# Optimization experiments

Hardware: AMD Instinct MI355X
Metric: run time of the kernel (lower is better)

Reference implementation:

```python
import jax, jax.numpy as jnp
import numpy as np

B, C, T = 16, 192, 4096
K = 5
L = 16


def conv1d(x, w, b, pad):
    # x: [B, Cin, T], w: [Cout, Cin, K] -> [B, Cout, T]
    y = jax.lax.conv_general_dilated(
        x, w, window_strides=(1,), padding=[(pad, pad)],
        dimension_numbers=("NCH", "OIH", "NCH"))
    return y + b[None, :, None]


def setup_inputs() -> dict:
    key = jax.random.key(0)
    ks = jax.random.split(key, 8)
    scale = 0.1
    x = jax.random.normal(ks[0], (B, C, T), dtype=jnp.float32)
    mask = jnp.ones((B, 1, T), dtype=jnp.float32)
    # in_layers: Conv1d(C -> 2C, K), stacked over layers (weight-norm folded)
    W_in = jax.random.normal(ks[1], (L, 2 * C, C, K), dtype=jnp.float32) * scale
    b_in = jax.random.normal(ks[2], (L, 2 * C), dtype=jnp.float32) * scale
    # res_skip layers 0..L-2: Conv1d(C -> 2C, 1)
    W_rs = jax.random.normal(ks[3], (L - 1, 2 * C, C, 1), dtype=jnp.float32) * scale
    b_rs = jax.random.normal(ks[4], (L - 1, 2 * C), dtype=jnp.float32) * scale
    # last res_skip layer: Conv1d(C -> C, 1)
    W_last = jax.random.normal(ks[5], (C, C, 1), dtype=jnp.float32) * scale
    b_last = jax.random.normal(ks[6], (C,), dtype=jnp.float32) * scale
    return {"x": x, "mask": mask, "W_in": W_in, "b_in": b_in,
            "W_rs": W_rs, "b_rs": b_rs, "W_last": W_last, "b_last": b_last}


def reference(x, mask, W_in, b_in, W_rs, b_rs, W_last, b_last):
    pad = K // 2  # dilation_rate == 1, so padding is 'same'
    o = jnp.zeros_like(x)
    for i in range(L):
        x_in = conv1d(x, W_in[i], b_in[i], pad)          # [B, 2C, T]
        x1, x2 = x_in[:, :C], x_in[:, C:]
        acts = jnp.tanh(x1) * jax.nn.sigmoid(x2)          # gated activation (dropout=0)
        if i == L - 1:
            o = o + conv1d(acts, W_last, b_last, 0)
        else:
            rs = conv1d(acts, W_rs[i], b_rs[i], 0)        # [B, 2C, T]
            x = (x + rs[:, :C]) * mask                    # residual
            o = o + rs[:, C:]                              # skip
    return o * mask
```

## Files before the change

kernel.cpp:

```cpp
#include <hip/hip_runtime.h>
#include <hip/hip_bf16.h>

#define C 192
#define T 4096
#define L 16
#define BATCH 16
#define NT 64
#define XR 72
#define CPAD 200

#define CONV_TAP_STRIDE 73728
#define MT_STRIDE       3072
#define ICC_STRIDE      512

typedef __attribute__((ext_vector_type(8))) _Float16 half8;
typedef __attribute__((ext_vector_type(4))) _Float16 half4;
typedef __attribute__((ext_vector_type(4))) float f32x4;

__device__ __forceinline__ float gatefn(float x1, float x2) {
    float ax = fabsf(x1);
    float e  = __expf(-2.f * ax);
    float th = __builtin_copysignf((1.f - e) / (1.f + e), x1);
    float sg = 1.f / (1.f + __expf(-x2));
    return th * sg;
}

__global__ __launch_bounds__(256)
void fmt_win(const float* __restrict__ W, _Float16* __restrict__ dst, int total) {
    int gid = blockIdx.x * 256 + threadIdx.x;
    if (gid >= total) return;
    int lane = gid & 63; int r = gid >> 6;
    int icc = r % 6; r /= 6;
    int mt  = r % 24; r /= 24;
    int tap = r % 5;  int l = r / 5;
    int oc  = mt * 16 + (lane & 15);
    int ic0 = icc * 32 + (lane >> 4) * 8;
    const float* s = W + ((size_t)((l * 384 + oc) * 192 + ic0)) * 5 + tap;
    half8 v;
    #pragma unroll
    for (int i = 0; i < 8; ++i) v[i] = (_Float16)s[(size_t)i * 5];
    *reinterpret_cast<half8*>(dst + (size_t)gid * 8) = v;
}

__global__ __launch_bounds__(256)
void fmt_w11(const float* __restrict__ W, _Float16* __restrict__ dst, int mtc, int total) {
    int gid = blockIdx.x * 256 + threadIdx.x;
    if (gid >= total) return;
    int lane = gid & 63; int r = gid >> 6;
    int icc = r % 6; r /= 6;
    int mt  = r % mtc; int l = r / mtc;
    int oc  = mt * 16 + (lane & 15);
    int ic0 = icc * 32 + (lane >> 4) * 8;
    const float* s = W + (size_t)(l * (mtc * 16) + oc) * 192 + ic0;
    half8 v;
    #pragma unroll
    for (int i = 0; i < 8; ++i) v[i] = (_Float16)s[i];
    *reinterpret_cast<half8*>(dst + (size_t)gid * 8) = v;
}

__global__ __launch_bounds__(256)
void xpose(const float* __restrict__ x, _Float16* __restrict__ xh, _Float16* __restrict__ xl)
{
    __shared__ float tile[C][65];
    const int t0 = blockIdx.x * 64;
    const int b  = blockIdx.y;
    const float* xg = x + (size_t)b * C * T;
    for (int idx = threadIdx.x; idx < C * 16; idx += 256) {
        int ch = idx & 15, c = idx >> 4;
        f32x4 v = *reinterpret_cast<const f32x4*>(xg + (size_t)c * T + t0 + ch * 4);
        #pragma unroll
        for (int q = 0; q < 4; ++q) tile[c][ch * 4 + q] = v[q];
    }
    __syncthreads();
    for (int idx = threadIdx.x; idx < 64 * 24; idx += 256) {
        int cc = idx % 24, t = idx / 24;
        half8 h8, l8;
        #pragma unroll
        for (int i = 0; i < 8; ++i) {
            float v = tile[cc * 8 + i][t];
            _Float16 h = (_Float16)v;
            h8[i] = h;
            l8[i] = (_Float16)(v - (float)h);
        }
        size_t off = (size_t)b * T * C + (size_t)(t0 + t) * C + cc * 8;
        *reinterpret_cast<half8*>(xh + off) = h8;
        *reinterpret_cast<half8*>(xl + off) = l8;
    }
}

template<bool FIRST, bool LAST>
__global__ __launch_bounds__(256, 2)
void wnet_layer(const _Float16* __restrict__ xhin, const _Float16* __restrict__ xlin,
                _Float16* __restrict__ xhout, _Float16* __restrict__ xlout,
                const float* __restrict__ mask,
                const _Float16* __restrict__ wc,
                const float* __restrict__ bc,
                const _Float16* __restrict__ wr,
                const float* __restrict__ br,
                float* __restrict__ o)
{
    __shared__ __align__(16) _Float16 xhi[XR * CPAD];
    __shared__ __align__(16) _Float16 xlo[NT * CPAD];

    const int tid = threadIdx.x;
    const int t0  = blockIdx.x * NT;
    const int b   = blockIdx.y;

    {
        const _Float16* gh = xhin + (size_t)b * T * C;
        for (int idx = tid; idx < XR * 24; idx += 256) {
            int chunk = idx % 24;
            int r     = idx / 24;
            int t = t0 - 4 + r;
            half8 v = {};
            if (t >= 0 && t < T)
                v = *reinterpret_cast<const half8*>(gh + (size_t)t * C + chunk * 8);
            *reinterpret_cast<half8*>(&xhi[r * CPAD + chunk * 8]) = v;
        }
        if constexpr (!LAST) {
            const _Float16* gl = xlin + (size_t)b * T * C;
            for (int idx = tid; idx < NT * 24; idx += 256) {
                int chunk = idx % 24;
                int r     = idx / 24;
                half8 v = *reinterpret_cast<const half8*>(
                    gl + (size_t)(t0 + r) * C + chunk * 8);
                *reinterpret_cast<half8*>(&xlo[r * CPAD + chunk * 8]) = v;
            }
        }
    }
    __syncthreads();

    const int lane = tid & 63;
    const int wm   = tid >> 6;
    const int col  = lane & 15;
    const int sg   = lane >> 4;

    int wbase[6];
    #pragma unroll
    for (int q = 0; q < 6; ++q) {
        int h = q / 3, j = q % 3;
        int mt = h * 12 + wm * 3 + j;
        wbase[q] = mt * MT_STRIDE + lane * 8;
    }

    f32x4 acc[3][2][4];
    #pragma unroll
    for (int j = 0; j < 3; ++j)
    #pragma unroll
    for (int h = 0; h < 2; ++h) {
        f32x4 bv = *reinterpret_cast<const f32x4*>(bc + (h * 12 + wm * 3 + j) * 16 + sg * 4);
        #pragma unroll
        for (int p = 0; p < 4; ++p) acc[j][h][p] = bv;
    }

    half8 hA[6], hB[6];
    #pragma unroll
    for (int q = 0; q < 6; ++q)
        hA[q] = *reinterpret_cast<const half8*>(wc + wbase[q]);

    auto convstep = [&](int icc, half8 (&curH)[6], half8 (&nxtH)[6],
                        size_t tapoff, size_t ntapoff, int tap) {
        const size_t coff = tapoff + (size_t)icc * ICC_STRIDE;
        const size_t noff = (icc == 5) ? ntapoff : coff + ICC_STRIDE;
        #pragma unroll
        for (int q = 0; q < 6; ++q)
            nxtH[q] = *reinterpret_cast<const half8*>(wc + noff + wbase[q]);
        half8 bh[4];
        #pragma unroll
        for (int p = 0; p < 4; ++p) {
            int off = (p * 16 + col + tap + 2) * CPAD + icc * 32 + sg * 8;
            bh[p] = *reinterpret_cast<const half8*>(&xhi[off]);
        }
        __builtin_amdgcn_sched_barrier(0);
        __builtin_amdgcn_s_setprio(1);
        #pragma unroll
        for (int h = 0; h < 2; ++h)
        #pragma unroll
        for (int j = 0; j < 3; ++j)
        #pragma unroll
        for (int p = 0; p < 4; ++p)
            acc[j][h][p] = __builtin_amdgcn_mfma_f32_16x16x32_f16(
                curH[h * 3 + j], bh[p], acc[j][h][p], 0, 0, 0);
        __builtin_amdgcn_s_setprio(0);
    };

    for (int tap = 0; tap < 5; ++tap) {
        const size_t tapoff  = (size_t)tap * CONV_TAP_STRIDE;
        const size_t ntapoff = (size_t)(tap < 4 ? tap + 1 : 4) * CONV_TAP_STRIDE;
        #pragma unroll
        for (int ih = 0; ih < 3; ++ih) {
            convstep(2 * ih,     hA, hB, tapoff, ntapoff, tap);
            convstep(2 * ih + 1, hB, hA, tapoff, ntapoff, tap);
        }
    }

    half4 xresh[3][4];
    if constexpr (!LAST) {
        #pragma unroll
        for (int p = 0; p < 4; ++p) {
            const int row = p * 16 + col + 4;
            #pragma unroll
            for (int j = 0; j < 3; ++j) {
                const int ch = (wm * 3 + j) * 16 + sg * 4;
                xresh[j][p] = *reinterpret_cast<const half4*>(&xhi[row * CPAD + ch]);
            }
        }
    }
    __syncthreads();

    #pragma unroll
    for (int j = 0; j < 3; ++j)
    #pragma unroll
    for (int p = 0; p < 4; ++p) {
        const int tt = p * 16 + col;
        const int ch = (wm * 3 + j) * 16 + sg * 4;
        half4 av;
        #pragma unroll
        for (int i = 0; i < 4; ++i)
            av[i] = (_Float16)gatefn(acc[j][0][p][i], acc[j][1][p][i]);
        *reinterpret_cast<half4*>(&xhi[tt * CPAD + ch]) = av;
    }
    __syncthreads();

    const float* mb = mask + (size_t)b * T;
    float mv[4];
    #pragma unroll
    for (int p = 0; p < 4; ++p) mv[p] = mb[t0 + p * 16 + col];

    constexpr int HN = LAST ? 1 : 2;
    constexpr int NQ = HN * 3;
    f32x4 a2[3][HN][4];
    #pragma unroll
    for (int j = 0; j < 3; ++j)
    #pragma unroll
    for (int h = 0; h < HN; ++h) {
        f32x4 bv = *reinterpret_cast<const f32x4*>(br + (h * 12 + wm * 3 + j) * 16 + sg * 4);
        #pragma unroll
        for (int p = 0; p < 4; ++p) a2[j][h][p] = bv;
    }

    half8 rA[NQ], rB[NQ];
    #pragma unroll
    for (int q = 0; q < NQ; ++q)
        rA[q] = *reinterpret_cast<const half8*>(wr + wbase[q]);

    auto r1step = [&](int icc, half8 (&cur)[NQ], half8 (&nxt)[NQ]) {
        const size_t noff = (size_t)(icc < 5 ? icc + 1 : 5) * ICC_STRIDE;
        #pragma unroll
        for (int q = 0; q < NQ; ++q)
            nxt[q] = *reinterpret_cast<const half8*>(wr + noff + wbase[q]);
        half8 bah[4];
        #pragma unroll
        for (int p = 0; p < 4; ++p) {
            int off = (p * 16 + col) * CPAD + icc * 32 + sg * 8;
            bah[p] = *reinterpret_cast<const half8*>(&xhi[off]);
        }
        __builtin_amdgcn_sched_barrier(0);
        __builtin_amdgcn_s_setprio(1);
        #pragma unroll
        for (int h = 0; h < HN; ++h)
        #pragma unroll
        for (int j = 0; j < 3; ++j)
        #pragma unroll
        for (int p = 0; p < 4; ++p)
            a2[j][h][p] = __builtin_amdgcn_mfma_f32_16x16x32_f16(
                cur[h * 3 + j], bah[p], a2[j][h][p], 0, 0, 0);
        __builtin_amdgcn_s_setprio(0);
    };

    #pragma unroll
    for (int ih = 0; ih < 3; ++ih) {
        r1step(2 * ih,     rA, rB);
        r1step(2 * ih + 1, rB, rA);
    }

    #pragma unroll
    for (int p = 0; p < 4; ++p) {
        const int tt = p * 16 + col;
        const int t  = t0 + tt;
        #pragma unroll
        for (int j = 0; j < 3; ++j) {
            const int ch = (wm * 3 + j) * 16 + sg * 4;
            if constexpr (LAST) {
                float* op = o + ((size_t)b * C + ch) * T + t;
                #pragma unroll
                for (int i = 0; i < 4; ++i)
                    op[(size_t)i * T] = (op[(size_t)i * T] + a2[j][0][p][i]) * mv[p];
            } else {
                size_t off = (size_t)b * T * C + (size_t)t * C + ch;
                half4 xl4 = *reinterpret_cast<const half4*>(&xlo[tt * CPAD + ch]);
                half4 h4, l4;
                #pragma unroll
                for (int i = 0; i < 4; ++i) {
                    float xm = (float)xresh[j][p][i] + (float)xl4[i];
                    float nx = (xm + a2[j][0][p][i]) * mv[p];
                    _Float16 hh = (_Float16)nx;
                    h4[i] = hh;
                    l4[i] = (_Float16)(nx - (float)hh);
                }
                *reinterpret_cast<half4*>(xhout + off) = h4;
                *reinterpret_cast<half4*>(xlout + off) = l4;
                float* op = o + ((size_t)b * C + ch) * T + t;
                #pragma unroll
                for (int i = 0; i < 4; ++i) {
                    if constexpr (FIRST) op[(size_t)i * T] = a2[j][1][p][i];
                    else                 op[(size_t)i * T] += a2[j][1][p][i];
                }
            }
        }
    }
}

#define WIN_STRIDE ((size_t)5 * 24 * 6 * 64 * 8)
#define WRS_STRIDE ((size_t)24 * 6 * 64 * 8)

extern "C" void kernel_launch(void* const* d_in, const int* in_sizes, int n_in,
                              void* d_out, int out_size, void* d_ws, size_t ws_size,
                              hipStream_t stream)
{
    const float* x      = (const float*)d_in[0];
    const float* mask   = (const float*)d_in[1];
    const float* W_in   = (const float*)d_in[2];
    const float* b_in   = (const float*)d_in[3];
    const float* W_rs   = (const float*)d_in[4];
    const float* b_rs   = (const float*)d_in[5];
    const float* W_last = (const float*)d_in[6];
    const float* b_last = (const float*)d_in[7];
    float* o = (float*)d_out;

    const size_t WIN_N = (size_t)L * WIN_STRIDE;
    const size_t WRS_N = (size_t)(L - 1) * WRS_STRIDE;
    const size_t WL_N  = (size_t)12 * 6 * 64 * 8;
    const size_t P     = (size_t)BATCH * T * C;
    _Float16* wc  = (_Float16*)d_ws;
    _Float16* wr  = wc + WIN_N;
    _Float16* wl  = wr + WRS_N;
    _Float16* xah = wl + WL_N;
    _Float16* xal = xah + P;
    _Float16* xbh = xal + P;
    _Float16* xbl = xbh + P;

    {
        int tw = (int)(L * 5 * 24 * 6 * 64);
        fmt_win<<<(tw + 255) / 256, 256, 0, stream>>>(W_in, wc, tw);
        int tr = (int)((L - 1) * 24 * 6 * 64);
        fmt_w11<<<(tr + 255) / 256, 256, 0, stream>>>(W_rs, wr, 24, tr);
        int tl = (int)(12 * 6 * 64);
        fmt_w11<<<(tl + 255) / 256, 256, 0, stream>>>(W_last, wl, 12, tl);
        xpose<<<dim3(T / 64, BATCH), 256, 0, stream>>>(x, xah, xal);
    }

    dim3 grid(T / NT, BATCH);
    dim3 block(256);

    _Float16* curh = xah; _Float16* curl = xal;
    _Float16* nxth = xbh; _Float16* nxtl = xbl;

    wnet_layer<true, false><<<grid, block, 0, stream>>>(
        curh, curl, nxth, nxtl, mask,
        wc, b_in, wr, b_rs, o);
    { _Float16* t1 = curh; curh = nxth; nxth = t1;
      _Float16* t2 = curl; curl = nxtl; nxtl = t2; }

    for (int i = 1; i < L - 1; ++i) {
        wnet_layer<false, false><<<grid, block, 0, stream>>>(
            curh, curl, nxth, nxtl, mask,
            wc + (size_t)i * WIN_STRIDE, b_in + (size_t)i * 2 * C,
            wr + (size_t)i * WRS_STRIDE, b_rs + (size_t)i * 2 * C, o);
        { _Float16* t1 = curh; curh = nxth; nxth = t1;
          _Float16* t2 = curl; curl = nxtl; nxtl = t2; }
    }

    wnet_layer<false, true><<<grid, block, 0, stream>>>(
        curh, curl, nullptr, nullptr, mask,
        wc + (size_t)(L - 1) * WIN_STRIDE, b_in + (size_t)(L - 1) * 2 * C,
        wl, b_last, o);
}
```

Baseline: 1.337 ms.

## Accumulate skip output in time-major layout and transpose at the end

Each layer's skip accumulator o is now stored time-major ([B,T,C]), so every thread reads and writes contiguous 4-float vectors instead of four scalars strided by T. A final transpose kernel converts o back to channel-major into a scratch buffer, and a linear copy writes it back into the output. The aim is to remove uncoalesced read-modify-write traffic across all 16 layers, at the cost of two extra full passes over the output.

Result: slower. 1.420 ms (+6.2%).

```diff
diff --git a/kernel.cpp b/kernel.cpp
--- a/kernel.cpp
+++ b/kernel.cpp
@@ -86,6 +86,39 @@
         *reinterpret_cast<half8*>(xh + off) = h8;
         *reinterpret_cast<half8*>(xl + off) = l8;
     }
+}
+
+__global__ __launch_bounds__(256)
+void o_t2c(const float* __restrict__ src, float* __restrict__ dst)
+{
+    __shared__ float tile[64][C + 1];
+    const int t0 = blockIdx.x * 64;
+    const int b  = blockIdx.y;
+    const float* s = src + (size_t)b * T * C;
+    for (int idx = threadIdx.x; idx < 64 * 48; idx += 256) {
+        int cc = idx % 48, tt = idx / 48;
+        f32x4 v = *reinterpret_cast<const f32x4*>(s + (size_t)(t0 + tt) * C + cc * 4);
+        #pragma unroll
+        for (int q = 0; q < 4; ++q) tile[tt][cc * 4 + q] = v[q];
+    }
+    __syncthreads();
+    float* d = dst + (size_t)b * C * T;
+    for (int idx = threadIdx.x; idx < C * 16; idx += 256) {
+        int g = idx % 16, c = idx / 16;
+        f32x4 w;
+        #pragma unroll
+        for (int q = 0; q < 4; ++q) w[q] = tile[g * 4 + q][c];
+        *reinterpret_cast<f32x4*>(d + (size_t)c * T + t0 + g * 4) = w;
+    }
+}
+
+__global__ __launch_bounds__(256)
+void copy_lin(const float* __restrict__ src, float* __restrict__ dst, long n4)
+{
+    long i = (long)blockIdx.x * 256 + threadIdx.x;
+    const long stride = (long)gridDim.x * 256;
+    for (; i < n4; i += stride)
+        reinterpret_cast<f32x4*>(dst)[i] = reinterpret_cast<const f32x4*>(src)[i];
 }
 
 template<bool FIRST, bool LAST>
@@ -281,13 +314,13 @@
         #pragma unroll
         for (int j = 0; j < 3; ++j) {
             const int ch = (wm * 3 + j) * 16 + sg * 4;
+            const size_t oo = (size_t)b * T * C + (size_t)t * C + ch;
             if constexpr (LAST) {
-                float* op = o + ((size_t)b * C + ch) * T + t;
+                f32x4 ov = *reinterpret_cast<const f32x4*>(o + oo);
                 #pragma unroll
-                for (int i = 0; i < 4; ++i)
-                    op[(size_t)i * T] = (op[(size_t)i * T] + a2[j][0][p][i]) * mv[p];
+                for (int i = 0; i < 4; ++i) ov[i] = (ov[i] + a2[j][0][p][i]) * mv[p];
+                *reinterpret_cast<f32x4*>(o + oo) = ov;
             } else {
-                size_t off = (size_t)b * T * C + (size_t)t * C + ch;
                 half4 xl4 = *reinterpret_cast<const half4*>(&xlo[tt * CPAD + ch]);
                 half4 h4, l4;
                 #pragma unroll
@@ -298,13 +331,15 @@
                     h4[i] = hh;
                     l4[i] = (_Float16)(nx - (float)hh);
                 }
-                *reinterpret_cast<half4*>(xhout + off) = h4;
-                *reinterpret_cast<half4*>(xlout + off) = l4;
-                float* op = o + ((size_t)b * C + ch) * T + t;
-                #pragma unroll
-                for (int i = 0; i < 4; ++i) {
-                    if constexpr (FIRST) op[(size_t)i * T] = a2[j][1][p][i];
-                    else                 op[(size_t)i * T] += a2[j][1][p][i];
+                *reinterpret_cast<half4*>(xhout + oo) = h4;
+                *reinterpret_cast<half4*>(xlout + oo) = l4;
+                if constexpr (FIRST) {
+                    *reinterpret_cast<f32x4*>(o + oo) = a2[j][1][p];
+                } else {
+                    f32x4 ov = *reinterpret_cast<const f32x4*>(o + oo);
+                    #pragma unroll
+                    for (int i = 0; i < 4; ++i) ov[i] += a2[j][1][p][i];
+                    *reinterpret_cast<f32x4*>(o + oo) = ov;
                 }
             }
         }
@@ -375,4 +410,8 @@
         curh, curl, nullptr, nullptr, mask,
         wc + (size_t)(L - 1) * WIN_STRIDE, b_in + (size_t)(L - 1) * 2 * C,
         wl, b_last, o);
-}
+
+    float* scratch = (float*)xah;
+    o_t2c<<<dim3(T / 64, BATCH), 256, 0, stream>>>(o, scratch);
+    copy_lin<<<1024, 256, 0, stream>>>(scratch, o, (long)(P / 4));
+}
```
